# Performance work log

Hardware: AMD Instinct MI355X
Metric: run time of the kernel (lower is better)

The kernel has to match this reference:

```python
import jax, jax.numpy as jnp
import numpy as np

B, N, IN_DIM, DIM, KNN = 8, 2048, 128, 128, 16
POS_H = 64
ATTN_H = DIM * 4
EPS = 1e-5
SCALE = 1.0 / np.sqrt(DIM).astype(np.float32)


def setup_inputs() -> dict:
    key = jax.random.key(0)
    ks = jax.random.split(key, 10)
    nrm = lambda k, shape, s=0.02: jax.random.normal(k, shape, jnp.float32) * s
    return dict(
        ori_x=jax.random.normal(ks[0], (B, N, IN_DIM), jnp.float32),
        pos=jax.random.normal(ks[1], (B, N, 3), jnp.float32),
        w_in=nrm(ks[2], (IN_DIM, DIM)),
        w_qkv=nrm(ks[3], (DIM, 3 * DIM)),
        w_out=nrm(ks[4], (DIM, IN_DIM)),
        pos_w1=nrm(ks[5], (3, POS_H)), pos_b1=jnp.zeros((POS_H,), jnp.float32),
        pos_bn_g=jnp.ones((POS_H,), jnp.float32), pos_bn_b=jnp.zeros((POS_H,), jnp.float32),
        pos_bn_m=jnp.zeros((POS_H,), jnp.float32), pos_bn_v=jnp.ones((POS_H,), jnp.float32),
        pos_w2=nrm(ks[6], (POS_H, DIM)), pos_b2=jnp.zeros((DIM,), jnp.float32),
        attn_w1=nrm(ks[7], (DIM, ATTN_H)), attn_b1=jnp.zeros((ATTN_H,), jnp.float32),
        attn_bn_g=jnp.ones((ATTN_H,), jnp.float32), attn_bn_b=jnp.zeros((ATTN_H,), jnp.float32),
        attn_bn_m=jnp.zeros((ATTN_H,), jnp.float32), attn_bn_v=jnp.ones((ATTN_H,), jnp.float32),
        attn_w2=nrm(ks[8], (ATTN_H, DIM)), attn_b2=jnp.zeros((DIM,), jnp.float32),
    )


def _bn_eval(x, g, b, m, v):
    # BatchNorm2d in eval mode; channel is the last axis in our [b,n,k,C] layout
    return (x - m) * (g * jax.lax.rsqrt(v + EPS)) + b


def reference(ori_x, pos, w_in, w_qkv, w_out,
              pos_w1, pos_b1, pos_bn_g, pos_bn_b, pos_bn_m, pos_bn_v, pos_w2, pos_b2,
              attn_w1, attn_b1, attn_bn_g, attn_bn_b, attn_bn_m, attn_bn_v, attn_w2, attn_b2):
    x = ori_x @ w_in                                  # [b,n,dim]
    qkv = x @ w_qkv
    q, k, v = jnp.split(qkv, 3, axis=-1)              # each [b,n,dim]

    # pairwise squared distances [b,n,n] (monotone in rel_dist -> same topk)
    sq = jnp.sum(pos * pos, axis=-1)
    d2 = sq[:, :, None] + sq[:, None, :] - 2.0 * jnp.einsum('bnd,bmd->bnm', pos, pos)
    _, idx = jax.lax.top_k(-d2, KNN)                  # [b,n,KNN] nearest neighbors

    gather = jax.vmap(lambda t, i: t[i])              # [n,C],[n,k] -> [n,k,C] per batch
    k_g = gather(k, idx)                              # [b,n,k,dim]
    v_g = gather(v, idx)
    pos_g = gather(pos, idx)                          # [b,n,k,3]

    rel_pos = pos[:, :, None, :] - pos_g              # [b,n,k,3]
    pe = jax.nn.relu(_bn_eval(rel_pos @ pos_w1 + pos_b1, pos_bn_g, pos_bn_b, pos_bn_m, pos_bn_v))
    pe = pe @ pos_w2 + pos_b2                         # [b,n,k,dim]

    qk_rel = q[:, :, None, :] - k_g                   # [b,n,k,dim]
    h = jax.nn.relu(_bn_eval((qk_rel + pe) @ attn_w1 + attn_b1,
                             attn_bn_g, attn_bn_b, attn_bn_m, attn_bn_v))
    h = h @ attn_w2 + attn_b2                         # [b,n,k,dim]

    attn = jax.nn.softmax(h * SCALE, axis=-2)         # softmax over neighbors
    agg = jnp.sum(attn * (v_g + pe), axis=2)          # [b,n,dim]
    return agg @ w_out + ori_x
```

## Files before the change

kernel.cpp:

```cpp
#include <hip/hip_runtime.h>

#define EPS 1e-5f

constexpr int NB   = 8;
constexpr int NN   = 2048;
constexpr int DIM  = 128;
constexpr int KNN  = 16;
constexpr int AH   = 512;
constexpr int NPTS = NB * NN;
constexpr float SCALE = 0.08838834764831845f;

typedef __attribute__((ext_vector_type(8))) short short8;
typedef __attribute__((ext_vector_type(4))) float floatx4;

__device__ __forceinline__ short f2bf(float f) {
  union { float f; unsigned u; } a; a.f = f;
  return (short)((a.u + 0x8000u) >> 16);
}
__device__ __forceinline__ float bf2f(short s) {
  union { unsigned u; float f; } a; a.u = ((unsigned)(unsigned short)s) << 16;
  return a.f;
}

__global__ __launch_bounds__(256) void pack_weights(
    const float* __restrict__ attn_w1, const float* __restrict__ attn_w2,
    const float* __restrict__ pos_w2, const float* __restrict__ w_in,
    const float* __restrict__ w_qkv,
    const float* __restrict__ w_out, const float* __restrict__ pos,
    const float* __restrict__ attn_b1, const float* __restrict__ abn_g,
    const float* __restrict__ abn_b, const float* __restrict__ abn_m,
    const float* __restrict__ abn_v,
    const float* __restrict__ pos_b1, const float* __restrict__ pbn_g,
    const float* __restrict__ pbn_b, const float* __restrict__ pbn_m,
    const float* __restrict__ pbn_v, const float* __restrict__ pos_b2,
    short* __restrict__ w1p, short* __restrict__ w2p, short* __restrict__ pw2p,
    short* __restrict__ wfp, short* __restrict__ wop,
    float* __restrict__ biasq,
    float* __restrict__ t1sc, float* __restrict__ t1bi,
    float* __restrict__ phsc, float* __restrict__ phbi,
    float* __restrict__ pos_t)
{
  int t = blockIdx.x * 256 + threadIdx.x;
  if (t < 65536) {
    int j = t & 7, lane = (t >> 3) & 63, ks = (t >> 9) & 3, nt = (t >> 11) & 3, ch = t >> 13;
    int q = lane >> 4, cc = lane & 15;
    int k = ks * 32 + q * 8 + j, n = ch * 64 + nt * 16 + cc;
    w1p[t] = f2bf(attn_w1[(size_t)k * AH + n]);
  } else if (t < 131072) {
    int e = t - 65536;
    int j = e & 7, lane = (e >> 3) & 63, ks = (e >> 9) & 1, nt = (e >> 10) & 7, ch = e >> 13;
    int q = lane >> 4, cc = lane & 15;
    int k = ch * 64 + ks * 32 + q * 8 + j, n = nt * 16 + cc;
    w2p[e] = f2bf(attn_w2[(size_t)k * DIM + n]);
  } else if (t < 139264) {
    int e = t - 131072;
    int j = e & 7, lane = (e >> 3) & 63, ks = (e >> 9) & 1, nt = e >> 10;
    int q = lane >> 4, cc = lane & 15;
    int k = ks * 32 + q * 8 + j, n = nt * 16 + cc;
    pw2p[e] = f2bf(pos_w2[(size_t)k * DIM + n]);
  } else if (t < 188416) {
    int e = t - 139264;
    int j = e & 7, lane = (e >> 3) & 63, ks = (e >> 9) & 3, nt = (e >> 11) & 7, nc = e >> 14;
    int q = lane >> 4, cc = lane & 15;
    int k = ks * 32 + q * 8 + j, n = nc * 128 + nt * 16 + cc;
    float s = 0.0f;
#pragma unroll 8
    for (int m = 0; m < 128; ++m)
      s += w_in[(size_t)k * DIM + m] * w_qkv[(size_t)m * 384 + n];
    wfp[e] = f2bf(s);
  } else if (t < 204800) {
    int e = t - 188416;
    int j = e & 7, lane = (e >> 3) & 63, ks = (e >> 9) & 3, nt = (e >> 11) & 7;
    int q = lane >> 4, cc = lane & 15;
    int k = ks * 32 + q * 8 + j, n = nt * 16 + cc;
    wop[e] = f2bf(w_out[(size_t)k * DIM + n]);
  } else if (t < 205184) {
    int c = t - 204800;
    biasq[c] = (c < 128) ? pos_b2[c] : ((c < 256) ? 0.0f : pos_b2[c - 256]);
  } else if (t < 205696) {
    int c = t - 205184;
    t1sc[c] = abn_g[c] * rsqrtf(abn_v[c] + EPS);
  } else if (t < 206208) {
    int c = t - 205696;
    float sc = abn_g[c] * rsqrtf(abn_v[c] + EPS);
    t1bi[c] = (attn_b1[c] - abn_m[c]) * sc + abn_b[c];
  } else if (t < 206272) {
    int c = t - 206208;
    phsc[c] = pbn_g[c] * rsqrtf(pbn_v[c] + EPS);
  } else if (t < 206336) {
    int c = t - 206272;
    float sc = pbn_g[c] * rsqrtf(pbn_v[c] + EPS);
    phbi[c] = (pos_b1[c] - pbn_m[c]) * sc + pbn_b[c];
  } else if (t < 206336 + NPTS * 3) {
    int e = t - 206336;
    int p = e / 3, d = e - p * 3;
    int b = p >> 11, n = p & (NN - 1);
    pos_t[((size_t)b * 3 + d) * NN + n] = pos[e];
  }
}

__global__ __launch_bounds__(256, 4) void knn_gemm_in(
    const float* __restrict__ A, const short* __restrict__ wfp,
    const float* __restrict__ biasq, short* __restrict__ C,
    const float* __restrict__ pos_t, int* __restrict__ idx_out)
{
  __shared__ short As[64 * 128];
  const int tid = threadIdx.x;
  const int bx = blockIdx.x;

  if (bx % 17 == 0) {
    const int lane = tid & 63, w = tid >> 6;
    const int wr = w >> 1, wc = w & 1;
    const int q = lane >> 4, cc = lane & 15;
    const int row0 = (bx / 17) * 64;
#pragma unroll
    for (int it = 0; it < 4; ++it) {
      int e = tid + it * 256;
      int row = e >> 4, cg = e & 15;
      const float* src = A + (size_t)(row0 + row) * 128 + cg * 8;
      float4 f0 = *(const float4*)src, f1 = *(const float4*)(src + 4);
      short8 v;
      v[0] = f2bf(f0.x); v[1] = f2bf(f0.y); v[2] = f2bf(f0.z); v[3] = f2bf(f0.w);
      v[4] = f2bf(f1.x); v[5] = f2bf(f1.y); v[6] = f2bf(f1.z); v[7] = f2bf(f1.w);
      *(short8*)(As + row * 128 + ((cg ^ (row & 15)) << 3)) = v;
    }
    __syncthreads();
    for (int nc = 0; nc < 3; ++nc) {
      floatx4 acc[2][4];
#pragma unroll
      for (int i = 0; i < 2; ++i)
#pragma unroll
        for (int jt = 0; jt < 4; ++jt) acc[i][jt] = (floatx4){0.f, 0.f, 0.f, 0.f};
#pragma unroll
      for (int ks = 0; ks < 4; ++ks) {
        short8 a8[2], b8[4];
#pragma unroll
        for (int i = 0; i < 2; ++i) {
          int row = (wr * 2 + i) * 16 + cc;
          a8[i] = *(const short8*)(As + row * 128 + (((ks * 4 + q) ^ cc) << 3));
        }
#pragma unroll
        for (int jt = 0; jt < 4; ++jt)
          b8[jt] = *(const short8*)(wfp + ((((nc * 8 + wc * 4 + jt) * 4 + ks) * 64 + lane) << 3));
#pragma unroll
        for (int i = 0; i < 2; ++i)
#pragma unroll
          for (int jt = 0; jt < 4; ++jt)
            acc[i][jt] = __builtin_amdgcn_mfma_f32_16x16x32_bf16(a8[i], b8[jt], acc[i][jt], 0, 0, 0);
      }
#pragma unroll
      for (int jt = 0; jt < 4; ++jt) {
        int colG = nc * 128 + (wc * 4 + jt) * 16 + cc;
        float bv = biasq[colG];
#pragma unroll
        for (int i = 0; i < 2; ++i)
#pragma unroll
          for (int r = 0; r < 4; ++r) {
            int row = (wr * 2 + i) * 16 + q * 4 + r;
            C[(size_t)(row0 + row) * 384 + colG] = f2bf(acc[i][jt][r] + bv);
          }
      }
    }
  } else {
    const int kb = bx - bx / 17 - 1;
    const int lane = tid & 63;
    const int p = kb * 4 + (tid >> 6);
    const int b = p >> 11, i = p & (NN - 1);
    const float* px = pos_t + (size_t)b * 3 * NN;
    const float* py = px + NN;
    const float* pz = py + NN;
    const float xi = px[i], yi = py[i], zi = pz[i];
    const float sqi = xi * xi + yi * yi + zi * zi;
    float v[32];
#pragma unroll
    for (int t = 0; t < 32; ++t) {
      int j = t * 64 + lane;
      float xj = px[j], yj = py[j], zj = pz[j];
      float sqj = xj * xj + yj * yj + zj * zj;
      float dot = xi * xj + yi * yj + zi * zj;
      v[t] = sqi + sqj - 2.0f * dot;
    }
    for (int s = 0; s < KNN; ++s) {
      float bv = 3.4e38f; int bj = 1 << 30;
#pragma unroll
      for (int t = 0; t < 32; ++t) {
        if (v[t] < bv) { bv = v[t]; bj = t * 64 + lane; }
      }
#pragma unroll
      for (int m = 1; m < 64; m <<= 1) {
        float ov = __shfl_xor(bv, m);
        int   oj = __shfl_xor(bj, m);
        if (ov < bv || (ov == bv && oj < bj)) { bv = ov; bj = oj; }
      }
      if (lane == 0) idx_out[(size_t)p * KNN + s] = bj;
#pragma unroll
      for (int t = 0; t < 32; ++t)
        if (bj == t * 64 + lane) v[t] = 3.4e38f;
    }
  }
}

__global__ __launch_bounds__(256, 3) void fused_attn(
    const float* __restrict__ pos_t, const short* __restrict__ qkv,
    const int* __restrict__ knn_idx,
    const float* __restrict__ pos_w1,
    const short* __restrict__ w1p, const short* __restrict__ w2p,
    const short* __restrict__ pw2p, const short* __restrict__ wop,
    const float* __restrict__ t1sc, const float* __restrict__ t1bi,
    const float* __restrict__ phsc, const float* __restrict__ phbi,
    const float* __restrict__ attn_b2,
    const float* __restrict__ ori_x, float* __restrict__ out)
{
  __shared__ short a_s[64 * 128];
  __shared__ short vpe_s[64 * 128];
  __shared__ short t1_s[2][64 * 64];
  __shared__ short q_ss[4 * 128];
  __shared__ float relp_s[64 * 4];
  __shared__ int   nbr_s[64];

  const int tid = threadIdx.x;
  const int lane = tid & 63, w = tid >> 6;
  const int wr = w >> 1, wc = w & 1;
  const int q = lane >> 4, cc = lane & 15;
  const int bb = blockIdx.x & 7;
  const int base = (blockIdx.x >> 3) * 4;
  const int gp0 = bb * NN + base;

  const float* px = pos_t + (size_t)bb * 3 * NN;
  const float* py = px + NN;
  const float* pz = py + NN;

  if (tid < 64) nbr_s[tid] = knn_idx[(size_t)gp0 * KNN + tid];
  else if (tid < 128) {
    int e = tid - 64;
    int p = e >> 4, seg = e & 15;
    *(short8*)(q_ss + p * 128 + seg * 8) =
        *(const short8*)(qkv + (size_t)(gp0 + p) * 384 + seg * 8);
  }
  __syncthreads();
  if (tid < 64) {
    int p = tid >> 4;
    int j = nbr_s[tid];
    relp_s[tid * 4 + 0] = px[base + p] - px[j];
    relp_s[tid * 4 + 1] = py[base + p] - py[j];
    relp_s[tid * 4 + 2] = pz[base + p] - pz[j];
  }
  __syncthreads();

#pragma unroll
  for (int r2 = 0; r2 < 16; ++r2) {
    int e = tid + r2 * 256;
    int row = e >> 6, c = e & 63;
    float lin = relp_s[row * 4] * pos_w1[c] + relp_s[row * 4 + 1] * pos_w1[64 + c]
              + relp_s[row * 4 + 2] * pos_w1[128 + c];
    t1_s[0][row * 64 + (((c >> 3) ^ (row & 7)) << 3) + (c & 7)] =
        f2bf(fmaxf(lin * phsc[c] + phbi[c], 0.0f));
  }
  __syncthreads();

  floatx4 pe[2][4];
#pragma unroll
  for (int i = 0; i < 2; ++i)
#pragma unroll
    for (int jt = 0; jt < 4; ++jt) pe[i][jt] = (floatx4){0.f, 0.f, 0.f, 0.f};
#pragma unroll
  for (int ks = 0; ks < 2; ++ks) {
    short8 a8[2];
#pragma unroll
    for (int i = 0; i < 2; ++i) {
      int row = (wr * 2 + i) * 16 + cc;
      a8[i] = *(const short8*)(t1_s[0] + row * 64 + (((ks * 4 + q) ^ (row & 7)) << 3));
    }
#pragma unroll
    for (int jt = 0; jt < 4; ++jt) {
      short8 b8 = *(const short8*)(pw2p + ((((wc * 4 + jt) * 2 + ks) * 64 + lane) << 3));
#pragma unroll
      for (int i = 0; i < 2; ++i)
        pe[i][jt] = __builtin_amdgcn_mfma_f32_16x16x32_bf16(a8[i], b8, pe[i][jt], 0, 0, 0);
    }
  }

#pragma unroll
  for (int i = 0; i < 2; ++i) {
    int rt = wr * 2 + i;
#pragma unroll
    for (int jt = 0; jt < 4; ++jt) {
      int col = (wc * 4 + jt) * 16 + cc;
      float qv = bf2f(q_ss[rt * 128 + col]);
#pragma unroll
      for (int r = 0; r < 4; ++r) {
        int row = rt * 16 + q * 4 + r;
        const short* kv = qkv + ((size_t)bb * NN + nbr_s[row]) * 384;
        float pev = pe[i][jt][r];
        int slot = row * 128 + (((col >> 3) ^ (row & 15)) << 3) + (col & 7);
        a_s[slot]   = f2bf(qv - bf2f(kv[128 + col]) + pev);
        vpe_s[slot] = f2bf(bf2f(kv[256 + col]) + pev);
      }
    }
  }
  __syncthreads();

  floatx4 hacc[2][4];
#pragma unroll
  for (int i = 0; i < 2; ++i)
#pragma unroll
    for (int jt = 0; jt < 4; ++jt) hacc[i][jt] = (floatx4){0.f, 0.f, 0.f, 0.f};

  for (int ch = 0; ch < 8; ++ch) {
    short* t1b = t1_s[ch & 1];
    floatx4 tacc[2][2];
#pragma unroll
    for (int i = 0; i < 2; ++i)
#pragma unroll
      for (int jt = 0; jt < 2; ++jt) tacc[i][jt] = (floatx4){0.f, 0.f, 0.f, 0.f};
#pragma unroll
    for (int ks = 0; ks < 4; ++ks) {
      short8 a8[2], b8[2];
#pragma unroll
      for (int i = 0; i < 2; ++i) {
        int row = (wr * 2 + i) * 16 + cc;
        a8[i] = *(const short8*)(a_s + row * 128 + (((ks * 4 + q) ^ cc) << 3));
      }
#pragma unroll
      for (int jt = 0; jt < 2; ++jt)
        b8[jt] = *(const short8*)(w1p + ((((ch * 4 + wc * 2 + jt) * 4 + ks) * 64 + lane) << 3));
#pragma unroll
      for (int i = 0; i < 2; ++i)
#pragma unroll
        for (int jt = 0; jt < 2; ++jt)
          tacc[i][jt] = __builtin_amdgcn_mfma_f32_16x16x32_bf16(a8[i], b8[jt], tacc[i][jt], 0, 0, 0);
    }
#pragma unroll
    for (int jt = 0; jt < 2; ++jt) {
      int colL = (wc * 2 + jt) * 16 + cc;
      int colG = ch * 64 + colL;
      float sc = t1sc[colG], bi = t1bi[colG];
#pragma unroll
      for (int i = 0; i < 2; ++i)
#pragma unroll
        for (int r = 0; r < 4; ++r) {
          int row = (wr * 2 + i) * 16 + q * 4 + r;
          t1b[row * 64 + (((colL >> 3) ^ (row & 7)) << 3) + (colL & 7)] =
              f2bf(fmaxf(tacc[i][jt][r] * sc + bi, 0.0f));
        }
    }
    __syncthreads();
#pragma unroll
    for (int ks = 0; ks < 2; ++ks) {
      short8 a8[2], b8[4];
#pragma unroll
      for (int i = 0; i < 2; ++i) {
        int row = (wr * 2 + i) * 16 + cc;
        a8[i] = *(const short8*)(t1b + row * 64 + (((ks * 4 + q) ^ (row & 7)) << 3));
      }
#pragma unroll
      for (int jt = 0; jt < 4; ++jt)
        b8[jt] = *(const short8*)(w2p + ((((ch * 8 + wc * 4 + jt) * 2 + ks) * 64 + lane) << 3));
#pragma unroll
      for (int i = 0; i < 2; ++i)
#pragma unroll
        for (int jt = 0; jt < 4; ++jt)
          hacc[i][jt] = __builtin_amdgcn_mfma_f32_16x16x32_bf16(a8[i], b8[jt], hacc[i][jt], 0, 0, 0);
    }
  }

  short* agg_s = t1_s[0];
#pragma unroll
  for (int r2 = 0; r2 < 6; ++r2) {
    int e = tid + r2 * 256;
    agg_s[(4 + (e >> 7)) * 128 + (e & 127)] = 0;
  }
#pragma unroll
  for (int i = 0; i < 2; ++i) {
    int rt = wr * 2 + i;
#pragma unroll
    for (int jt = 0; jt < 4; ++jt) {
      int col = (wc * 4 + jt) * 16 + cc;
      float b2v = attn_b2[col];
      float v0[4], mx = -3.4e38f;
#pragma unroll
      for (int r = 0; r < 4; ++r) {
        v0[r] = (hacc[i][jt][r] + b2v) * SCALE;
        mx = fmaxf(mx, v0[r]);
      }
      mx = fmaxf(mx, __shfl_xor(mx, 16));
      mx = fmaxf(mx, __shfl_xor(mx, 32));
      float ex[4], sum = 0.f;
#pragma unroll
      for (int r = 0; r < 4; ++r) { ex[r] = __expf(v0[r] - mx); sum += ex[r]; }
      sum += __shfl_xor(sum, 16);
      sum += __shfl_xor(sum, 32);
      float inv = 1.0f / sum;
      float part = 0.f;
#pragma unroll
      for (int r = 0; r < 4; ++r) {
        int row = rt * 16 + q * 4 + r;
        int slot = row * 128 + (((col >> 3) ^ (row & 15)) << 3) + (col & 7);
        part += ex[r] * bf2f(vpe_s[slot]);
      }
      part += __shfl_xor(part, 16);
      part += __shfl_xor(part, 32);
      if (q == 0) agg_s[rt * 128 + col] = f2bf(part * inv);
    }
  }
  __syncthreads();

  {
    floatx4 oacc[2];
#pragma unroll
    for (int jt = 0; jt < 2; ++jt) oacc[jt] = (floatx4){0.f, 0.f, 0.f, 0.f};
#pragma unroll
    for (int ks = 0; ks < 4; ++ks) {
      short8 a8 = *(const short8*)(agg_s + cc * 128 + ks * 32 + q * 8);
#pragma unroll
      for (int jt = 0; jt < 2; ++jt) {
        short8 b8 = *(const short8*)(wop + ((((w * 2 + jt) * 4 + ks) * 64 + lane) << 3));
        oacc[jt] = __builtin_amdgcn_mfma_f32_16x16x32_bf16(a8, b8, oacc[jt], 0, 0, 0);
      }
    }
    if (q == 0) {
#pragma unroll
      for (int jt = 0; jt < 2; ++jt) {
        int col = (w * 2 + jt) * 16 + cc;
#pragma unroll
        for (int r = 0; r < 4; ++r) {
          size_t o = (size_t)(gp0 + r) * 128 + col;
          out[o] = oacc[jt][r] + ori_x[o];
        }
      }
    }
  }
}

extern "C" void kernel_launch(void* const* d_in, const int* in_sizes, int n_in,
                              void* d_out, int out_size, void* d_ws, size_t ws_size,
                              hipStream_t stream)
{
  const float* ori_x    = (const float*)d_in[0];
  const float* pos      = (const float*)d_in[1];
  const float* w_in     = (const float*)d_in[2];
  const float* w_qkv    = (const float*)d_in[3];
  const float* w_out    = (const float*)d_in[4];
  const float* pos_w1   = (const float*)d_in[5];
  const float* pos_b1   = (const float*)d_in[6];
  const float* pos_bn_g = (const float*)d_in[7];
  const float* pos_bn_b = (const float*)d_in[8];
  const float* pos_bn_m = (const float*)d_in[9];
  const float* pos_bn_v = (const float*)d_in[10];
  const float* pos_w2   = (const float*)d_in[11];
  const float* pos_b2   = (const float*)d_in[12];
  const float* attn_w1  = (const float*)d_in[13];
  const float* attn_b1  = (const float*)d_in[14];
  const float* attn_bn_g = (const float*)d_in[15];
  const float* attn_bn_b = (const float*)d_in[16];
  const float* attn_bn_m = (const float*)d_in[17];
  const float* attn_bn_v = (const float*)d_in[18];
  const float* attn_w2  = (const float*)d_in[19];
  const float* attn_b2  = (const float*)d_in[20];
  float* out = (float*)d_out;

  short* qkvb = (short*)d_ws;
  short* w1p  = qkvb + (size_t)NPTS * 3 * DIM;
  short* w2p  = w1p + 65536;
  short* pw2p = w2p + 65536;
  short* wfp  = pw2p + 8192;
  short* wop  = wfp + 49152;
  float* biasq = (float*)(wop + 16384);
  float* t1sc = biasq + 384;
  float* t1bi = t1sc + 512;
  float* phsc = t1bi + 512;
  float* phbi = phsc + 64;
  float* pos_t = phbi + 64;
  int*   idx  = (int*)(pos_t + (size_t)NB * 3 * NN);

  pack_weights<<<998, 256, 0, stream>>>(attn_w1, attn_w2, pos_w2, w_in, w_qkv,
      w_out, pos,
      attn_b1, attn_bn_g, attn_bn_b, attn_bn_m, attn_bn_v,
      pos_b1, pos_bn_g, pos_bn_b, pos_bn_m, pos_bn_v, pos_b2,
      w1p, w2p, pw2p, wfp, wop, biasq, t1sc, t1bi, phsc, phbi, pos_t);
  knn_gemm_in<<<4352, 256, 0, stream>>>(ori_x, wfp, biasq, qkvb, pos_t, idx);
  fused_attn<<<NPTS / 4, 256, 0, stream>>>(pos_t, qkvb, idx, pos_w1,
      w1p, w2p, pw2p, wop, t1sc, t1bi, phsc, phbi, attn_b2, ori_x, out);
}
```

Baseline: 366.1 us.

## Coalesce weight packing, double kNN queries per wave, stage neighbor K/V rows

```diff
diff --git a/kernel.cpp b/kernel.cpp
--- a/kernel.cpp
+++ b/kernel.cpp
@@ -42,22 +42,26 @@
 {
   int t = blockIdx.x * 256 + threadIdx.x;
   if (t < 65536) {
-    int j = t & 7, lane = (t >> 3) & 63, ks = (t >> 9) & 3, nt = (t >> 11) & 3, ch = t >> 13;
-    int q = lane >> 4, cc = lane & 15;
-    int k = ks * 32 + q * 8 + j, n = ch * 64 + nt * 16 + cc;
-    w1p[t] = f2bf(attn_w1[(size_t)k * AH + n]);
+    int k = t >> 9, n = t & 511;
+    int ks = k >> 5, q = (k >> 3) & 3, j = k & 7;
+    int ch = n >> 6, nt = (n >> 4) & 3, cc = n & 15;
+    int dst = ch * 8192 + nt * 2048 + ks * 512 + (q * 16 + cc) * 8 + j;
+    w1p[dst] = f2bf(attn_w1[t]);
   } else if (t < 131072) {
-    int e = t - 65536;
-    int j = e & 7, lane = (e >> 3) & 63, ks = (e >> 9) & 1, nt = (e >> 10) & 7, ch = e >> 13;
-    int q = lane >> 4, cc = lane & 15;
-    int k = ch * 64 + ks * 32 + q * 8 + j, n = nt * 16 + cc;
-    w2p[e] = f2bf(attn_w2[(size_t)k * DIM + n]);
+    int s = t - 65536;
+    int k = s >> 7, n = s & 127;
+    int ch = k >> 6, r = k & 63;
+    int ks = r >> 5, q = (r >> 3) & 3, j = r & 7;
+    int nt = n >> 4, cc = n & 15;
+    int dst = ch * 8192 + nt * 1024 + ks * 512 + (q * 16 + cc) * 8 + j;
+    w2p[dst] = f2bf(attn_w2[s]);
   } else if (t < 139264) {
-    int e = t - 131072;
-    int j = e & 7, lane = (e >> 3) & 63, ks = (e >> 9) & 1, nt = e >> 10;
-    int q = lane >> 4, cc = lane & 15;
-    int k = ks * 32 + q * 8 + j, n = nt * 16 + cc;
-    pw2p[e] = f2bf(pos_w2[(size_t)k * DIM + n]);
+    int s = t - 131072;
+    int k = s >> 7, n = s & 127;
+    int ks = k >> 5, r = k & 31, q = r >> 3, j = r & 7;
+    int nt = n >> 4, cc = n & 15;
+    int dst = nt * 1024 + ks * 512 + (q * 16 + cc) * 8 + j;
+    pw2p[dst] = f2bf(pos_w2[s]);
   } else if (t < 188416) {
     int e = t - 139264;
     int j = e & 7, lane = (e >> 3) & 63, ks = (e >> 9) & 3, nt = (e >> 11) & 7, nc = e >> 14;
@@ -69,11 +73,12 @@
       s += w_in[(size_t)k * DIM + m] * w_qkv[(size_t)m * 384 + n];
     wfp[e] = f2bf(s);
   } else if (t < 204800) {
-    int e = t - 188416;
-    int j = e & 7, lane = (e >> 3) & 63, ks = (e >> 9) & 3, nt = (e >> 11) & 7;
-    int q = lane >> 4, cc = lane & 15;
-    int k = ks * 32 + q * 8 + j, n = nt * 16 + cc;
-    wop[e] = f2bf(w_out[(size_t)k * DIM + n]);
+    int s = t - 188416;
+    int k = s >> 7, n = s & 127;
+    int ks = k >> 5, q = (k >> 3) & 3, j = k & 7;
+    int nt = n >> 4, cc = n & 15;
+    int dst = nt * 2048 + ks * 512 + (q * 16 + cc) * 8 + j;
+    wop[dst] = f2bf(w_out[s]);
   } else if (t < 205184) {
     int c = t - 204800;
     biasq[c] = (c < 128) ? pos_b2[c] : ((c < 256) ? 0.0f : pos_b2[c - 256]);
@@ -108,11 +113,11 @@
   const int tid = threadIdx.x;
   const int bx = blockIdx.x;
 
-  if (bx % 17 == 0) {
+  if (bx % 9 == 0) {
     const int lane = tid & 63, w = tid >> 6;
     const int wr = w >> 1, wc = w & 1;
     const int q = lane >> 4, cc = lane & 15;
-    const int row0 = (bx / 17) * 64;
+    const int row0 = (bx / 9) * 64;
 #pragma unroll
     for (int it = 0; it < 4; ++it) {
       int e = tid + it * 256;
@@ -162,40 +167,50 @@
       }
     }
   } else {
-    const int kb = bx - bx / 17 - 1;
+    const int kb = bx - bx / 9 - 1;
     const int lane = tid & 63;
-    const int p = kb * 4 + (tid >> 6);
-    const int b = p >> 11, i = p & (NN - 1);
+    const int p0 = kb * 8 + (tid >> 6) * 2;
+    const int b = p0 >> 11, i0 = p0 & (NN - 1), i1 = i0 + 1;
     const float* px = pos_t + (size_t)b * 3 * NN;
     const float* py = px + NN;
     const float* pz = py + NN;
-    const float xi = px[i], yi = py[i], zi = pz[i];
-    const float sqi = xi * xi + yi * yi + zi * zi;
-    float v[32];
+    const float xa = px[i0], ya = py[i0], za = pz[i0];
+    const float sqa = xa * xa + ya * ya + za * za;
+    const float xb = px[i1], yb = py[i1], zb = pz[i1];
+    const float sqb = xb * xb + yb * yb + zb * zb;
+    float va[32], vb[32];
 #pragma unroll
     for (int t = 0; t < 32; ++t) {
       int j = t * 64 + lane;
       float xj = px[j], yj = py[j], zj = pz[j];
       float sqj = xj * xj + yj * yj + zj * zj;
-      float dot = xi * xj + yi * yj + zi * zj;
-      v[t] = sqi + sqj - 2.0f * dot;
+      va[t] = sqa + sqj - 2.0f * (xa * xj + ya * yj + za * zj);
+      vb[t] = sqb + sqj - 2.0f * (xb * xj + yb * yj + zb * zj);
     }
     for (int s = 0; s < KNN; ++s) {
+      float av = 3.4e38f; int aj = 1 << 30;
       float bv = 3.4e38f; int bj = 1 << 30;
 #pragma unroll
       for (int t = 0; t < 32; ++t) {
-        if (v[t] < bv) { bv = v[t]; bj = t * 64 + lane; }
+        if (va[t] < av) { av = va[t]; aj = t * 64 + lane; }
+        if (vb[t] < bv) { bv = vb[t]; bj = t * 64 + lane; }
       }
 #pragma unroll
       for (int m = 1; m < 64; m <<= 1) {
-        float ov = __shfl_xor(bv, m);
-        int   oj = __shfl_xor(bj, m);
-        if (ov < bv || (ov == bv && oj < bj)) { bv = ov; bj = oj; }
-      }
-      if (lane == 0) idx_out[(size_t)p * KNN + s] = bj;
-#pragma unroll
-      for (int t = 0; t < 32; ++t)
-        if (bj == t * 64 + lane) v[t] = 3.4e38f;
+        float oav = __shfl_xor(av, m); int oaj = __shfl_xor(aj, m);
+        float obv = __shfl_xor(bv, m); int obj = __shfl_xor(bj, m);
+        if (oav < av || (oav == av && oaj < aj)) { av = oav; aj = oaj; }
+        if (obv < bv || (obv == bv && obj < bj)) { bv = obv; bj = obj; }
+      }
+      if (lane == 0) {
+        idx_out[(size_t)p0 * KNN + s] = aj;
+        idx_out[(size_t)(p0 + 1) * KNN + s] = bj;
+      }
+#pragma unroll
+      for (int t = 0; t < 32; ++t) {
+        if (aj == t * 64 + lane) va[t] = 3.4e38f;
+        if (bj == t * 64 + lane) vb[t] = 3.4e38f;
+      }
     }
   }
 }
@@ -281,6 +296,17 @@
   }
 
 #pragma unroll
+  for (int it = 0; it < 4; ++it) {
+    int e = tid + it * 256;
+    int row = e >> 4, g = e & 15;
+    const short* kvrow = qkv + ((size_t)bb * NN + nbr_s[row]) * 384;
+    int dst = row * 128 + ((g ^ (row & 15)) << 3);
+    *(short8*)(a_s + dst)   = *(const short8*)(kvrow + 128 + g * 8);
+    *(short8*)(vpe_s + dst) = *(const short8*)(kvrow + 256 + g * 8);
+  }
+  __syncthreads();
+
+#pragma unroll
   for (int i = 0; i < 2; ++i) {
     int rt = wr * 2 + i;
 #pragma unroll
@@ -290,11 +316,10 @@
 #pragma unroll
       for (int r = 0; r < 4; ++r) {
         int row = rt * 16 + q * 4 + r;
-        const short* kv = qkv + ((size_t)bb * NN + nbr_s[row]) * 384;
         float pev = pe[i][jt][r];
         int slot = row * 128 + (((col >> 3) ^ (row & 15)) << 3) + (col & 7);
-        a_s[slot]   = f2bf(qv - bf2f(kv[128 + col]) + pev);
-        vpe_s[slot] = f2bf(bf2f(kv[256 + col]) + pev);
+        a_s[slot]   = f2bf(qv - bf2f(a_s[slot]) + pev);
+        vpe_s[slot] = f2bf(bf2f(vpe_s[slot]) + pev);
       }
     }
   }
@@ -366,11 +391,6 @@
 
   short* agg_s = t1_s[0];
 #pragma unroll
-  for (int r2 = 0; r2 < 6; ++r2) {
-    int e = tid + r2 * 256;
-    agg_s[(4 + (e >> 7)) * 128 + (e & 127)] = 0;
-  }
-#pragma unroll
   for (int i = 0; i < 2; ++i) {
     int rt = wr * 2 + i;
 #pragma unroll
@@ -400,7 +420,7 @@
       }
       part += __shfl_xor(part, 16);
       part += __shfl_xor(part, 32);
-      if (q == 0) agg_s[rt * 128 + col] = f2bf(part * inv);
+      if (q == 0) agg_s[rt * 136 + col] = f2bf(part * inv);
     }
   }
   __syncthreads();
@@ -411,7 +431,7 @@
     for (int jt = 0; jt < 2; ++jt) oacc[jt] = (floatx4){0.f, 0.f, 0.f, 0.f};
 #pragma unroll
     for (int ks = 0; ks < 4; ++ks) {
-      short8 a8 = *(const short8*)(agg_s + cc * 128 + ks * 32 + q * 8);
+      short8 a8 = *(const short8*)(agg_s + cc * 136 + ks * 32 + q * 8);
 #pragma unroll
       for (int jt = 0; jt < 2; ++jt) {
         short8 b8 = *(const short8*)(wop + ((((w * 2 + jt) * 4 + ks) * 64 + lane) << 3));
@@ -478,7 +498,7 @@
       attn_b1, attn_bn_g, attn_bn_b, attn_bn_m, attn_bn_v,
       pos_b1, pos_bn_g, pos_bn_b, pos_bn_m, pos_bn_v, pos_b2,
       w1p, w2p, pw2p, wfp, wop, biasq, t1sc, t1bi, phsc, phbi, pos_t);
-  knn_gemm_in<<<4352, 256, 0, stream>>>(ori_x, wfp, biasq, qkvb, pos_t, idx);
+  knn_gemm_in<<<2304, 256, 0, stream>>>(ori_x, wfp, biasq, qkvb, pos_t, idx);
   fused_attn<<<NPTS / 4, 256, 0, stream>>>(pos_t, qkvb, idx, pos_w1,
       w1p, w2p, pw2p, wop, t1sc, t1bi, phsc, phbi, attn_b2, ori_x, out);
 }
```

After: 361.9 us. About the same (-1.1%).
